# Kernel tuning notes

Measured on AMD Instinct MI355X. Metric: run time of the kernel, lower is better.

Reference implementation:

```python
import jax, jax.numpy as jnp
import numpy as np

NUM_HEAD = 8
GN_GROUPS = 32
EPS = 1e-5


def group_norm(x, w, b):
    # x: [B,C,H,W]; GroupNorm over 32 groups
    B, C, H, W = x.shape
    xg = x.reshape(B, GN_GROUPS, C // GN_GROUPS, H, W)
    mu = jnp.mean(xg, axis=(2, 3, 4), keepdims=True)
    var = jnp.var(xg, axis=(2, 3, 4), keepdims=True)
    xn = ((xg - mu) * jax.lax.rsqrt(var + EPS)).reshape(B, C, H, W)
    return xn * w[None, :, None, None] + b[None, :, None, None]


def conv1x1(x, w, b):
    # 1x1 conv == channel-wise linear: w [O,C], x [B,C,H,W]
    return jnp.einsum('oc,bchw->bohw', w, x) + b[None, :, None, None]


def setup_inputs() -> dict:
    key = jax.random.key(0)
    ks = jax.random.split(key, 6)
    B, C, H, W = 8, 512, 32, 32
    s = 1.0 / np.sqrt(C)
    return {
        'x': jax.random.normal(ks[0], (B, C, H, W), jnp.float32),
        'gn_w': jnp.ones((C,), jnp.float32),
        'gn_b': jnp.zeros((C,), jnp.float32),
        'wq': jax.random.normal(ks[1], (C, C), jnp.float32) * s,
        'bq': jnp.zeros((C,), jnp.float32),
        'wk': jax.random.normal(ks[2], (C, C), jnp.float32) * s,
        'bk': jnp.zeros((C,), jnp.float32),
        'wv': jax.random.normal(ks[3], (C, C), jnp.float32) * s,
        'bv': jnp.zeros((C,), jnp.float32),
        'wo': jax.random.normal(ks[4], (C, C), jnp.float32) * s,
        'bo': jnp.zeros((C,), jnp.float32),
    }


def reference(x, gn_w, gn_b, wq, bq, wk, bk, wv, bv, wo, bo):
    B, C, H, W = x.shape
    Hn = NUM_HEAD
    d = C // Hn
    N = H * W
    scale = d ** -0.5

    xn = group_norm(x, gn_w, gn_b)
    q = conv1x1(xn, wq, bq).reshape(B, Hn, d, N)  # [B,Hn,d,N]
    k = conv1x1(xn, wk, bk).reshape(B, Hn, d, N)
    v = conv1x1(xn, wv, bv).reshape(B, Hn, d, N)

    # attn[b,h,i,j] = sum_d q[b,h,d,i] * k[b,h,d,j]
    attn = jnp.einsum('bhdi,bhdj->bhij', q, k) * scale
    attn = jax.nn.softmax(attn, axis=-1)
    # out[b,h,d,i] = sum_j attn[b,h,i,j] * v[b,h,d,j]
    out = jnp.einsum('bhij,bhdj->bhdi', attn, v).reshape(B, C, H, W)
    return x + conv1x1(out, wo, bo)
```

## Files before the change

kernel.cpp:

```cpp
#include <hip/hip_runtime.h>
#include <hip/hip_bf16.h>

typedef unsigned short ushort_t;
typedef __bf16 bf16_t;
typedef bf16_t bf16x8 __attribute__((ext_vector_type(8)));
typedef float f32x4 __attribute__((ext_vector_type(4)));
typedef float f32x16 __attribute__((ext_vector_type(16)));

#define CH 512
#define NSP 1024

__device__ __forceinline__ float bf2f(ushort_t u) {
    union { unsigned int i; float f; } t; t.i = ((unsigned int)u) << 16; return t.f;
}
__device__ __forceinline__ ushort_t f2bf(float f) {
    union { float fl; unsigned int i; } t; t.fl = f;
    unsigned int r = t.i + 0x7fffu + ((t.i >> 16) & 1u);
    return (ushort_t)(r >> 16);
}
__device__ __forceinline__ unsigned int pk2(float a, float b) {
    __hip_bfloat162 h = __float22bfloat162_rn(make_float2(a, b));
    union { __hip_bfloat162 h2; unsigned int u; } t; t.h2 = h; return t.u;
}

#if __has_builtin(__builtin_amdgcn_global_load_lds)
#define HAVE_ASYNC_LDS 1
#endif
__device__ __forceinline__ void cp16(const ushort_t* g, ushort_t* l) {
#ifdef HAVE_ASYNC_LDS
    __builtin_amdgcn_global_load_lds((const __attribute__((address_space(1))) unsigned int*)g,
                                     (__attribute__((address_space(3))) unsigned int*)l, 16, 0, 0);
#else
    *(uint4*)l = *(const uint4*)g;
#endif
}

#if __has_builtin(__builtin_amdgcn_exp2f)
#define EXP2(x) __builtin_amdgcn_exp2f(x)
#else
#define EXP2(x) exp2f(x)
#endif

#define QSCALE 0.18033688011112042f

__global__ __launch_bounds__(256) void prep_w(const float* __restrict__ w0, const float* __restrict__ w1,
                                              const float* __restrict__ w2, const float* __restrict__ w3,
                                              ushort_t* __restrict__ wbf) {
    int idx = blockIdx.x * 256 + threadIdx.x;
    int my = idx >> 16;
    const float* src = (my == 0) ? w0 : (my == 1) ? w1 : (my == 2) ? w2 : w3;
    float4 v = reinterpret_cast<const float4*>(src)[idx & 65535];
    uint2 u = make_uint2(pk2(v.x, v.y), pk2(v.z, v.w));
    reinterpret_cast<uint2*>(wbf + (size_t)my * 262144)[idx & 65535] = u;
}

__global__ __launch_bounds__(256) void gn_fused(const float* __restrict__ x, const float* __restrict__ gw,
                                                const float* __restrict__ gbias,
                                                ushort_t* __restrict__ xnt) {
    __shared__ float red[8];
    int bg = blockIdx.x;
    int b = bg >> 5, g = bg & 31;
    int tid = threadIdx.x;
    const float4* x4 = reinterpret_cast<const float4*>(x + (size_t)bg * 16384);
    float4 v[16];
    float s = 0.f, s2 = 0.f;
    #pragma unroll
    for (int i = 0; i < 16; i++) {
        v[i] = x4[i * 256 + tid];
        s  += v[i].x + v[i].y + v[i].z + v[i].w;
        s2 += v[i].x * v[i].x + v[i].y * v[i].y + v[i].z * v[i].z + v[i].w * v[i].w;
    }
    #pragma unroll
    for (int off = 32; off > 0; off >>= 1) {
        s  += __shfl_down(s, off, 64);
        s2 += __shfl_down(s2, off, 64);
    }
    int wv = tid >> 6;
    if ((tid & 63) == 0) { red[wv] = s; red[4 + wv] = s2; }
    __syncthreads();
    float ts  = red[0] + red[1] + red[2] + red[3];
    float ts2 = red[4] + red[5] + red[6] + red[7];
    float mu  = ts * (1.f / 16384.f);
    float var = ts2 * (1.f / 16384.f) - mu * mu;
    float rstd = rsqrtf(var + 1e-5f);
    float ca[16], cb[16];
    #pragma unroll
    for (int cc = 0; cc < 16; cc++) {
        float ww = gw[g * 16 + cc], bb = gbias[g * 16 + cc];
        ca[cc] = rstd * ww; cb[cc] = bb - mu * ca[cc];
    }
    #pragma unroll
    for (int jj = 0; jj < 4; jj++) {
        float e[16];
        #pragma unroll
        for (int cc = 0; cc < 16; cc++) {
            float xv = (jj == 0) ? v[cc].x : (jj == 1) ? v[cc].y : (jj == 2) ? v[cc].z : v[cc].w;
            e[cc] = xv * ca[cc] + cb[cc];
        }
        uint4 u0 = make_uint4(pk2(e[0], e[1]), pk2(e[2], e[3]), pk2(e[4], e[5]), pk2(e[6], e[7]));
        uint4 u1 = make_uint4(pk2(e[8], e[9]), pk2(e[10], e[11]), pk2(e[12], e[13]), pk2(e[14], e[15]));
        ushort_t* dst = xnt + ((size_t)(b * 1024 + 4 * tid + jj)) * 512 + g * 16;
        *reinterpret_cast<uint4*>(dst)     = u0;
        *reinterpret_cast<uint4*>(dst + 8) = u1;
    }
}

__global__ __launch_bounds__(256) void conv_qkv(const ushort_t* __restrict__ xnt,
                                                const ushort_t* __restrict__ wbf,
                                                const float* __restrict__ bq,
                                                const float* __restrict__ bk,
                                                const float* __restrict__ bv,
                                                ushort_t* __restrict__ qt,
                                                ushort_t* __restrict__ kt,
                                                ushort_t* __restrict__ vt) {
    __shared__ __align__(16) char smem[17408];
// ... 51 lines not shown
        const float* bias = seg ? bk : bq;
        ushort_t* dst = seg ? kt : qt;
        float s = seg ? 1.f : QSCALE;
        float bv0 = bias[lo + wn * 32 + l15];
        float bv1 = bias[lo + wn * 32 + 16 + l15];
        ushort_t* cls = (ushort_t*)smem;
        #pragma unroll
        for (int ms = 0; ms < 4; ms++)
            #pragma unroll
            for (int ns = 0; ns < 2; ns++) {
                float bb = ns ? bv1 : bv0;
                int idx = (wm * 64 + ms * 16 + quad * 4) * 64 + wn * 32 + ns * 16 + l15;
                unsigned int ua = pk2((acc[ms][ns][0] + bb) * s, (acc[ms][ns][1] + bb) * s);
                unsigned int ub = pk2((acc[ms][ns][2] + bb) * s, (acc[ms][ns][3] + bb) * s);
                cls[idx]       = (ushort_t)(ua & 0xffff);
                cls[idx + 64]  = (ushort_t)(ua >> 16);
                cls[idx + 128] = (ushort_t)(ub & 0xffff);
                cls[idx + 192] = (ushort_t)(ub >> 16);
            }
        __syncthreads();
        int h = lo >> 6;
        size_t obase = ((size_t)(b * 8 + h) * 1024 + m0) * 64;
        #pragma unroll
        for (int rep = 0; rep < 4; rep++) {
            int id = rep * 256 + tid;
            int r = id >> 3, part = id & 7;
            *(uint4*)(dst + obase + (size_t)r * 64 + part * 8) = *(const uint4*)(cls + r * 64 + part * 8);
        }
    } else {
        float bv0 = bv[lo + wn * 32 + l15];
        float bv1 = bv[lo + wn * 32 + 16 + l15];
        ushort_t* clst = (ushort_t*)smem;
        #pragma unroll
        for (int ms = 0; ms < 4; ms++)
            #pragma unroll
            for (int ns = 0; ns < 2; ns++) {
                float bb = ns ? bv1 : bv0;
                unsigned int ua = pk2(acc[ms][ns][0] + bb, acc[ms][ns][1] + bb);
                unsigned int ub = pk2(acc[ms][ns][2] + bb, acc[ms][ns][3] + bb);
                *(uint2*)(&clst[(wn * 32 + ns * 16 + l15) * 136 + wm * 64 + ms * 16 + quad * 4]) =
                    make_uint2(ua, ub);
            }
        __syncthreads();
        #pragma unroll
        for (int rep = 0; rep < 4; rep++) {
            int id = rep * 256 + tid;
            int row = id >> 4, part = id & 15;
            *(uint4*)(vt + ((size_t)(b * 512 + lo + row) * 1024 + m0 + part * 8)) =
                *(const uint4*)(clst + row * 136 + part * 8);
        }
    }
}

#define Z16 {0.f,0.f,0.f,0.f,0.f,0.f,0.f,0.f,0.f,0.f,0.f,0.f,0.f,0.f,0.f,0.f}

#define PV_STEP(JS, P) {                                                                     \
    unsigned wA0 = pk2(P[((JS)&1)*8+0], P[((JS)&1)*8+1]);                                    \
    unsigned wA1 = pk2(P[((JS)&1)*8+2], P[((JS)&1)*8+3]);                                    \
    unsigned wB0 = pk2(P[((JS)&1)*8+4], P[((JS)&1)*8+5]);                                    \
    unsigned wB1 = pk2(P[((JS)&1)*8+6], P[((JS)&1)*8+7]);                                    \
    asm("v_permlane32_swap_b32 %0, %1" : "+v"(wA0), "+v"(wB0));                              \
    asm("v_permlane32_swap_b32 %0, %1" : "+v"(wA1), "+v"(wB1));                              \
    union { unsigned u[4]; bf16x8 v; } pa_;                                                  \
    pa_.u[0] = wA0; pa_.u[1] = wA1; pa_.u[2] = wB0; pa_.u[3] = wB1;                          \
    int phys_ = (((JS) * 2) | hi) ^ r7;                                                      \
    bf16x8 vf0 = *(const bf16x8*)(vbuf + l31 * 64 + phys_ * 8);                              \
    bf16x8 vf1 = *(const bf16x8*)(vbuf + (32 + l31) * 64 + phys_ * 8);                       \
    __builtin_amdgcn_s_setprio(1);                                                           \
    vacc0 = __builtin_amdgcn_mfma_f32_32x32x16_bf16(pa_.v, vf0, vacc0, 0, 0, 0);             \
    vacc1 = __builtin_amdgcn_mfma_f32_32x32x16_bf16(pa_.v, vf1, vacc1, 0, 0, 0);             \
    __builtin_amdgcn_s_setprio(0); }

__global__ __launch_bounds__(256) void attn_kernel(const ushort_t* __restrict__ qt,
                                                   const ushort_t* __restrict__ kt,
                                                   const ushort_t* __restrict__ vt,
                                                   ushort_t* __restrict__ ao) {
    __shared__ __align__(16) ushort_t smem[16384];
    int tid = threadIdx.x;
    int wave = tid >> 6, lane = tid & 63, l31 = lane & 31, hi = lane >> 5;
    int id = blockIdx.x;
    int bh = (id & 7) * 8 + (id >> 6);
    int i0 = ((id >> 3) & 7) * 128;
    const ushort_t* qb = qt + (size_t)bh * 65536;
    const ushort_t* kb = kt + (size_t)bh * 65536;
    const ushort_t* vb = vt + (size_t)bh * 65536;
    int iw0 = i0 + wave * 32;
    int r7 = l31 & 7;

    bf16x8 qf[4];
    #pragma unroll
    for (int ks = 0; ks < 4; ks++)
        qf[ks] = *(const bf16x8*)(qb + (size_t)(iw0 + l31) * 64 + ks * 16 + hi * 8);

    f32x16 vacc0 = Z16, vacc1 = Z16;
    float lacc = 0.f;

    int rk0 = tid >> 3, sk = tid & 7, rk1 = rk0 + 32;
    const ushort_t* kg0 = kb + rk0 * 64 + (sk ^ (rk0 & 7)) * 8;
    const ushort_t* kg1 = kb + rk1 * 64 + (sk ^ (rk1 & 7)) * 8;
    const ushort_t* vg0 = vb + (size_t)rk0 * 1024 + (sk ^ (rk0 & 7)) * 8;
    const ushort_t* vg1 = vb + (size_t)rk1 * 1024 + (sk ^ (rk1 & 7)) * 8;

    cp16(kg0, smem + tid * 8);
    cp16(kg1, smem + (tid + 256) * 8);
    cp16(vg0, smem + 8192 + tid * 8);
    cp16(vg1, smem + 8192 + (tid + 256) * 8);
    kg0 += 4096; kg1 += 4096; vg0 += 64; vg1 += 64;
    __syncthreads();

    for (int jt = 0; jt < 16; jt++) {
        int cur = jt & 1;
        if (jt < 15) {
            ushort_t* kd = smem + (cur ^ 1) * 4096;
            ushort_t* vd = smem + 8192 + (cur ^ 1) * 4096;
            cp16(kg0, kd + tid * 8);
            cp16(kg1, kd + (tid + 256) * 8);
            cp16(vg0, vd + tid * 8);
            cp16(vg1, vd + (tid + 256) * 8);
            kg0 += 4096; kg1 += 4096; vg0 += 64; vg1 += 64;
        }
        const ushort_t* kbuf = smem + cur * 4096;
        const ushort_t* vbuf = smem + 8192 + cur * 4096;

        f32x16 s0 = Z16, s1 = Z16;
        __builtin_amdgcn_s_setprio(1);
        #pragma unroll
        for (int ks = 0; ks < 4; ks++) {
            int phys = ((ks * 2) | hi) ^ r7;
            bf16x8 kf = *(const bf16x8*)(kbuf + l31 * 64 + phys * 8);
            s0 = __builtin_amdgcn_mfma_f32_32x32x16_bf16(kf, qf[ks], s0, 0, 0, 0);
        }
        #pragma unroll
        for (int ks = 0; ks < 4; ks++) {
            int phys = ((ks * 2) | hi) ^ r7;
            bf16x8 kf = *(const bf16x8*)(kbuf + (32 + l31) * 64 + phys * 8);
            s1 = __builtin_amdgcn_mfma_f32_32x32x16_bf16(kf, qf[ks], s1, 0, 0, 0);
        }
        __builtin_amdgcn_s_setprio(0);

        float p0[16], p1[16];
        #pragma unroll
        for (int r = 0; r < 16; r++) p0[r] = EXP2(s0[r]);
        #pragma unroll
        for (int r = 0; r < 16; r++) p1[r] = EXP2(s1[r]);
        float t0 = 0.f, t1 = 0.f, t2 = 0.f, t3 = 0.f;
        #pragma unroll
        for (int r = 0; r < 4; r++) { t0 += p0[r]; t1 += p0[4 + r]; t2 += p0[8 + r]; t3 += p0[12 + r]; }
        #pragma unroll
        for (int r = 0; r < 4; r++) { t0 += p1[r]; t1 += p1[4 + r]; t2 += p1[8 + r]; t3 += p1[12 + r]; }
        lacc += (t0 + t1) + (t2 + t3);

        PV_STEP(0, p0)
        PV_STEP(1, p0)
        PV_STEP(2, p1)
        PV_STEP(3, p1)

        __syncthreads();
    }

    lacc += __shfl_xor(lacc, 32, 64);
    float linv[16];
    #pragma unroll
    for (int r = 0; r < 16; r++) {
        int ir = (r & 3) + 8 * (r >> 2) + 4 * hi;
        linv[r] = 1.f / __shfl(lacc, ir, 64);
    }

    ushort_t* ols = smem;
    #pragma unroll
    for (int r = 0; r < 16; r++) {
        int irow = wave * 32 + (r & 3) + 8 * (r >> 2) + 4 * hi;
        ols[irow * 80 + l31]      = f2bf(vacc0[r] * linv[r]);
        ols[irow * 80 + 32 + l31] = f2bf(vacc1[r] * linv[r]);
    }
    __syncthreads();
    int b = bh >> 3, h = bh & 7;
    ushort_t* aob = ao + ((size_t)b * 1024 + i0) * 512 + h * 64;
    #pragma unroll
    for (int rep = 0; rep < 4; rep++) {
        int idd = rep * 256 + tid;
        int rl = idd >> 3, part = idd & 7;
        *(uint4*)(aob + (size_t)rl * 512 + part * 8) = *(const uint4*)(ols + rl * 80 + part * 8);
    }
}

__global__ __launch_bounds__(256) void conv_out(const ushort_t* __restrict__ ao,
                                                const ushort_t* __restrict__ wo,
                                                const float* __restrict__ bo,
                                                const float* __restrict__ xres,
                                                float* __restrict__ out) {
    __shared__ __align__(16) char smem[12288];
    ushort_t* als = (ushort_t*)smem;
    ushort_t* bls = (ushort_t*)(smem + 8192);
    int tid = threadIdx.x;
    int wave = tid >> 6, lane = tid & 63, l15 = lane & 15, quad = lane >> 4;
    int wm = wave >> 1, wn = wave & 1;
    int m0 = blockIdx.x * 128, o0 = blockIdx.y * 64, b = blockIdx.z;
    const ushort_t* A = ao + (size_t)b * 524288;

    f32x4 acc[4][2];
    #pragma unroll
    for (int ms = 0; ms < 4; ms++)
        #pragma unroll
        for (int ns = 0; ns < 2; ns++) acc[ms][ns] = (f32x4){0.f, 0.f, 0.f, 0.f};

    for (int k0 = 0; k0 < 512; k0 += 32) {
        #pragma unroll
        for (int rep = 0; rep < 2; rep++) {
            int id = rep * 256 + tid;
            int r = id >> 2, part = id & 3;
            int sw = part ^ ((r >> 2) & 3);
            cp16(A + (size_t)(m0 + r) * 512 + k0 + sw * 8, als + (size_t)id * 8);
        }
        {
            int r = tid >> 2, part = tid & 3;
            int sw = part ^ ((r >> 2) & 3);
            cp16(wo + (size_t)(o0 + r) * 512 + k0 + sw * 8, bls + (size_t)tid * 8);
        }
        __syncthreads();
        bf16x8 af[4], bfr[2];
        #pragma unroll
        for (int ms = 0; ms < 4; ms++) {
            int row = wm * 64 + ms * 16 + l15;
            int slot = quad ^ ((row >> 2) & 3);
            af[ms] = *(const bf16x8*)(als + row * 32 + slot * 8);
        }
        #pragma unroll
        for (int ns = 0; ns < 2; ns++) {
            int row = wn * 32 + ns * 16 + l15;
            int slot = quad ^ ((row >> 2) & 3);
            bfr[ns] = *(const bf16x8*)(bls + row * 32 + slot * 8);
        }
        #pragma unroll
        for (int ms = 0; ms < 4; ms++)
            #pragma unroll
            for (int ns = 0; ns < 2; ns++)
                acc[ms][ns] = __builtin_amdgcn_mfma_f32_16x16x32_bf16(af[ms], bfr[ns], acc[ms][ns], 0, 0, 0);
        __syncthreads();
    }

    #pragma unroll
    for (int ns = 0; ns < 2; ns++) {
        int o = o0 + wn * 32 + ns * 16 + l15;
        float bb = bo[o];
        #pragma unroll
        for (int ms = 0; ms < 4; ms++) {
            int n = m0 + wm * 64 + ms * 16 + quad * 4;
            size_t ga = ((size_t)(b * 512 + o)) * 1024 + n;
            float4 xv = *(const float4*)(xres + ga);
            float4 c4;
            c4.x = acc[ms][ns][0] + bb + xv.x;
            c4.y = acc[ms][ns][1] + bb + xv.y;
            c4.z = acc[ms][ns][2] + bb + xv.z;
            c4.w = acc[ms][ns][3] + bb + xv.w;
            *(float4*)(out + ga) = c4;
        }
    }
}

extern "C" void kernel_launch(void* const* d_in, const int* in_sizes, int n_in,
                              void* d_out, int out_size, void* d_ws, size_t ws_size,
                              hipStream_t stream) {
    const float* x    = (const float*)d_in[0];
    const float* gn_w = (const float*)d_in[1];
    const float* gn_b = (const float*)d_in[2];
    const float* wq   = (const float*)d_in[3];
    const float* bq   = (const float*)d_in[4];
    const float* wk   = (const float*)d_in[5];
    const float* bk   = (const float*)d_in[6];
    const float* wv   = (const float*)d_in[7];
    const float* bv   = (const float*)d_in[8];
    const float* wo   = (const float*)d_in[9];
    const float* bo   = (const float*)d_in[10];

    char* ws = (char*)d_ws;
    ushort_t* xnt  = (ushort_t*)(ws);
    ushort_t* qt   = (ushort_t*)(ws + (((size_t)8)  << 20));
    ushort_t* kt   = (ushort_t*)(ws + (((size_t)16) << 20));
    ushort_t* vt   = (ushort_t*)(ws + (((size_t)24) << 20));
    ushort_t* wbf  = (ushort_t*)(ws + (((size_t)32) << 20));
    ushort_t* ao   = xnt;

    prep_w<<<1024, 256, 0, stream>>>(wq, wk, wv, wo, wbf);
    gn_fused<<<256, 256, 0, stream>>>(x, gn_w, gn_b, xnt);

    conv_qkv<<<dim3(8, 24, 8), 256, 0, stream>>>(xnt, wbf, bq, bk, bv, qt, kt, vt);

    attn_kernel<<<512, 256, 0, stream>>>(qt, kt, vt, ao);

    conv_out<<<dim3(8, 8, 8), 256, 0, stream>>>(ao, wbf + 786432, bo, x, (float*)d_out);
}
```

Baseline: 159.9 us.

## Split attention key tiles across waves and halve query rows per block

Each attention block now processes 64 query rows with a 2x2 wave split over query rows and key halves, doubling the grid to 1024 blocks. Partial PV accumulators and row sums from the two key-half waves are reduced through shared memory before normalization and store. This is meant to raise parallelism and occupancy (with a launch-bounds hint of 4 blocks), at the cost of reloading K/V for twice as many blocks and an extra cross-wave reduction.

```diff
diff --git a/kernel.cpp b/kernel.cpp
--- a/kernel.cpp
+++ b/kernel.cpp
@@ -220,11 +220,11 @@
 
 #define Z16 {0.f,0.f,0.f,0.f,0.f,0.f,0.f,0.f,0.f,0.f,0.f,0.f,0.f,0.f,0.f,0.f}
 
-#define PV_STEP(JS, P) {                                                                     \
-    unsigned wA0 = pk2(P[((JS)&1)*8+0], P[((JS)&1)*8+1]);                                    \
-    unsigned wA1 = pk2(P[((JS)&1)*8+2], P[((JS)&1)*8+3]);                                    \
-    unsigned wB0 = pk2(P[((JS)&1)*8+4], P[((JS)&1)*8+5]);                                    \
-    unsigned wB1 = pk2(P[((JS)&1)*8+6], P[((JS)&1)*8+7]);                                    \
+#define PV_STEP(JS, PPTR) {                                                                  \
+    unsigned wA0 = pk2(PPTR[0], PPTR[1]);                                                    \
+    unsigned wA1 = pk2(PPTR[2], PPTR[3]);                                                    \
+    unsigned wB0 = pk2(PPTR[4], PPTR[5]);                                                    \
+    unsigned wB1 = pk2(PPTR[6], PPTR[7]);                                                    \
     asm("v_permlane32_swap_b32 %0, %1" : "+v"(wA0), "+v"(wB0));                              \
     asm("v_permlane32_swap_b32 %0, %1" : "+v"(wA1), "+v"(wB1));                              \
     union { unsigned u[4]; bf16x8 v; } pa_;                                                  \
@@ -237,21 +237,24 @@
     vacc1 = __builtin_amdgcn_mfma_f32_32x32x16_bf16(pa_.v, vf1, vacc1, 0, 0, 0);             \
     __builtin_amdgcn_s_setprio(0); }
 
-__global__ __launch_bounds__(256) void attn_kernel(const ushort_t* __restrict__ qt,
-                                                   const ushort_t* __restrict__ kt,
-                                                   const ushort_t* __restrict__ vt,
-                                                   ushort_t* __restrict__ ao) {
+__global__ __launch_bounds__(256, 4) void attn_kernel(const ushort_t* __restrict__ qt,
+                                                      const ushort_t* __restrict__ kt,
+                                                      const ushort_t* __restrict__ vt,
+                                                      ushort_t* __restrict__ ao) {
     __shared__ __align__(16) ushort_t smem[16384];
+    __shared__ float lred[128];
     int tid = threadIdx.x;
     int wave = tid >> 6, lane = tid & 63, l31 = lane & 31, hi = lane >> 5;
+    int wi = wave & 1, wj = wave >> 1;
     int id = blockIdx.x;
-    int bh = (id & 7) * 8 + (id >> 6);
-    int i0 = ((id >> 3) & 7) * 128;
+    int bh = (id & 7) * 8 + (id >> 7);
+    int i0 = ((id >> 3) & 15) * 64;
     const ushort_t* qb = qt + (size_t)bh * 65536;
     const ushort_t* kb = kt + (size_t)bh * 65536;
     const ushort_t* vb = vt + (size_t)bh * 65536;
-    int iw0 = i0 + wave * 32;
+    int iw0 = i0 + wi * 32;
     int r7 = l31 & 7;
+    int jrow = wj * 32 + l31;
 
     bf16x8 qf[4];
     #pragma unroll
@@ -288,62 +291,66 @@
         const ushort_t* kbuf = smem + cur * 4096;
         const ushort_t* vbuf = smem + 8192 + cur * 4096;
 
-        f32x16 s0 = Z16, s1 = Z16;
+        f32x16 s = Z16;
         __builtin_amdgcn_s_setprio(1);
         #pragma unroll
         for (int ks = 0; ks < 4; ks++) {
             int phys = ((ks * 2) | hi) ^ r7;
-            bf16x8 kf = *(const bf16x8*)(kbuf + l31 * 64 + phys * 8);
-            s0 = __builtin_amdgcn_mfma_f32_32x32x16_bf16(kf, qf[ks], s0, 0, 0, 0);
-        }
-        #pragma unroll
-        for (int ks = 0; ks < 4; ks++) {
-            int phys = ((ks * 2) | hi) ^ r7;
-            bf16x8 kf = *(const bf16x8*)(kbuf + (32 + l31) * 64 + phys * 8);
-            s1 = __builtin_amdgcn_mfma_f32_32x32x16_bf16(kf, qf[ks], s1, 0, 0, 0);
+            bf16x8 kf = *(const bf16x8*)(kbuf + jrow * 64 + phys * 8);
+            s = __builtin_amdgcn_mfma_f32_32x32x16_bf16(kf, qf[ks], s, 0, 0, 0);
         }
         __builtin_amdgcn_s_setprio(0);
 
-        float p0[16], p1[16];
-        #pragma unroll
-        for (int r = 0; r < 16; r++) p0[r] = EXP2(s0[r]);
-        #pragma unroll
-        for (int r = 0; r < 16; r++) p1[r] = EXP2(s1[r]);
+        float p[16];
+        #pragma unroll
+        for (int r = 0; r < 16; r++) p[r] = EXP2(s[r]);
         float t0 = 0.f, t1 = 0.f, t2 = 0.f, t3 = 0.f;
         #pragma unroll
-        for (int r = 0; r < 4; r++) { t0 += p0[r]; t1 += p0[4 + r]; t2 += p0[8 + r]; t3 += p0[12 + r]; }
-        #pragma unroll
-        for (int r = 0; r < 4; r++) { t0 += p1[r]; t1 += p1[4 + r]; t2 += p1[8 + r]; t3 += p1[12 + r]; }
+        for (int r = 0; r < 4; r++) { t0 += p[r]; t1 += p[4 + r]; t2 += p[8 + r]; t3 += p[12 + r]; }
         lacc += (t0 + t1) + (t2 + t3);
 
-        PV_STEP(0, p0)
-        PV_STEP(1, p0)
-        PV_STEP(2, p1)
-        PV_STEP(3, p1)
+        PV_STEP(wj * 2,     (p))
+        PV_STEP(wj * 2 + 1, (p + 8))
 
         __syncthreads();
     }
 
     lacc += __shfl_xor(lacc, 32, 64);
-    float linv[16];
-    #pragma unroll
-    for (int r = 0; r < 16; r++) {
-        int ir = (r & 3) + 8 * (r >> 2) + 4 * hi;
-        linv[r] = 1.f / __shfl(lacc, ir, 64);
-    }
-
-    ushort_t* ols = smem;
-    #pragma unroll
-    for (int r = 0; r < 16; r++) {
-        int irow = wave * 32 + (r & 3) + 8 * (r >> 2) + 4 * hi;
-        ols[irow * 80 + l31]      = f2bf(vacc0[r] * linv[r]);
-        ols[irow * 80 + 32 + l31] = f2bf(vacc1[r] * linv[r]);
+    lred[wave * 32 + l31] = lacc;
+
+    float* om = (float*)smem;
+    if (wj == 1) {
+        #pragma unroll
+        for (int r = 0; r < 16; r++) {
+            int row = wi * 32 + (r & 3) + 8 * (r >> 2) + 4 * hi;
+            om[row * 64 + l31]      = vacc0[r];
+            om[row * 64 + 32 + l31] = vacc1[r];
+        }
+    }
+    __syncthreads();
+    ushort_t* ols = smem + 8192;
+    if (wj == 0) {
+        float ltot = lacc + lred[(wave ^ 2) * 32 + l31];
+        float linv[16];
+        #pragma unroll
+        for (int r = 0; r < 16; r++) {
+            int ir = (r & 3) + 8 * (r >> 2) + 4 * hi;
+            linv[r] = 1.f / __shfl(ltot, ir, 64);
+        }
+        #pragma unroll
+        for (int r = 0; r < 16; r++) {
+            int row = wi * 32 + (r & 3) + 8 * (r >> 2) + 4 * hi;
+            float o0 = vacc0[r] + om[row * 64 + l31];
+            float o1 = vacc1[r] + om[row * 64 + 32 + l31];
+            ols[row * 80 + l31]      = f2bf(o0 * linv[r]);
+            ols[row * 80 + 32 + l31] = f2bf(o1 * linv[r]);
+        }
     }
     __syncthreads();
     int b = bh >> 3, h = bh & 7;
     ushort_t* aob = ao + ((size_t)b * 1024 + i0) * 512 + h * 64;
     #pragma unroll
-    for (int rep = 0; rep < 4; rep++) {
+    for (int rep = 0; rep < 2; rep++) {
         int idd = rep * 256 + tid;
         int rl = idd >> 3, part = idd & 7;
         *(uint4*)(aob + (size_t)rl * 512 + part * 8) = *(const uint4*)(ols + rl * 80 + part * 8);
@@ -452,7 +459,7 @@
 
     conv_qkv<<<dim3(8, 24, 8), 256, 0, stream>>>(xnt, wbf, bq, bk, bv, qt, kt, vt);
 
-    attn_kernel<<<512, 256, 0, stream>>>(qt, kt, vt, ao);
+    attn_kernel<<<1024, 256, 0, stream>>>(qt, kt, vt, ao);
 
     conv_out<<<dim3(8, 8, 8), 256, 0, stream>>>(ao, wbf + 786432, bo, x, (float*)d_out);
 }
```

Result: no change. 160.1 us (+0.1%).

## Split attention KV tile across wave pairs with 64-row query tiles per wave

Applied to the files above, without the earlier changes.

Each wave now handles 64 query rows against half of each 64-key tile, rather than 32 query rows against the full tile. Every K and V fragment read from LDS is therefore reused across two MFMAs, which cuts LDS read traffic per MFMA. The two partial outputs and row sums are combined through shared memory at the end. In exchange, accumulator register pressure doubles, a cross-wave reduction with extra barriers is added, and launch bounds request two blocks per CU.

```diff
diff --git a/kernel.cpp b/kernel.cpp
--- a/kernel.cpp
+++ b/kernel.cpp
@@ -220,46 +220,57 @@
 
 #define Z16 {0.f,0.f,0.f,0.f,0.f,0.f,0.f,0.f,0.f,0.f,0.f,0.f,0.f,0.f,0.f,0.f}
 
-#define PV_STEP(JS, P) {                                                                     \
-    unsigned wA0 = pk2(P[((JS)&1)*8+0], P[((JS)&1)*8+1]);                                    \
-    unsigned wA1 = pk2(P[((JS)&1)*8+2], P[((JS)&1)*8+3]);                                    \
-    unsigned wB0 = pk2(P[((JS)&1)*8+4], P[((JS)&1)*8+5]);                                    \
-    unsigned wB1 = pk2(P[((JS)&1)*8+6], P[((JS)&1)*8+7]);                                    \
-    asm("v_permlane32_swap_b32 %0, %1" : "+v"(wA0), "+v"(wB0));                              \
-    asm("v_permlane32_swap_b32 %0, %1" : "+v"(wA1), "+v"(wB1));                              \
-    union { unsigned u[4]; bf16x8 v; } pa_;                                                  \
-    pa_.u[0] = wA0; pa_.u[1] = wA1; pa_.u[2] = wB0; pa_.u[3] = wB1;                          \
+#define PV_STEP2(JS, PA, PB) {                                                               \
+    unsigned a0 = pk2(PA[0], PA[1]), a1 = pk2(PA[2], PA[3]);                                 \
+    unsigned a2 = pk2(PA[4], PA[5]), a3 = pk2(PA[6], PA[7]);                                 \
+    asm("v_permlane32_swap_b32 %0, %1" : "+v"(a0), "+v"(a2));                                \
+    asm("v_permlane32_swap_b32 %0, %1" : "+v"(a1), "+v"(a3));                                \
+    union { unsigned u[4]; bf16x8 v; } paA_;                                                 \
+    paA_.u[0] = a0; paA_.u[1] = a1; paA_.u[2] = a2; paA_.u[3] = a3;                          \
+    unsigned b0 = pk2(PB[0], PB[1]), b1 = pk2(PB[2], PB[3]);                                 \
+    unsigned b2 = pk2(PB[4], PB[5]), b3 = pk2(PB[6], PB[7]);                                 \
+    asm("v_permlane32_swap_b32 %0, %1" : "+v"(b0), "+v"(b2));                                \
+    asm("v_permlane32_swap_b32 %0, %1" : "+v"(b1), "+v"(b3));                                \
+    union { unsigned u[4]; bf16x8 v; } paB_;                                                 \
+    paB_.u[0] = b0; paB_.u[1] = b1; paB_.u[2] = b2; paB_.u[3] = b3;                          \
     int phys_ = (((JS) * 2) | hi) ^ r7;                                                      \
     bf16x8 vf0 = *(const bf16x8*)(vbuf + l31 * 64 + phys_ * 8);                              \
     bf16x8 vf1 = *(const bf16x8*)(vbuf + (32 + l31) * 64 + phys_ * 8);                       \
     __builtin_amdgcn_s_setprio(1);                                                           \
-    vacc0 = __builtin_amdgcn_mfma_f32_32x32x16_bf16(pa_.v, vf0, vacc0, 0, 0, 0);             \
-    vacc1 = __builtin_amdgcn_mfma_f32_32x32x16_bf16(pa_.v, vf1, vacc1, 0, 0, 0);             \
+    vacc0A = __builtin_amdgcn_mfma_f32_32x32x16_bf16(paA_.v, vf0, vacc0A, 0, 0, 0);          \
+    vacc1A = __builtin_amdgcn_mfma_f32_32x32x16_bf16(paA_.v, vf1, vacc1A, 0, 0, 0);          \
+    vacc0B = __builtin_amdgcn_mfma_f32_32x32x16_bf16(paB_.v, vf0, vacc0B, 0, 0, 0);          \
+    vacc1B = __builtin_amdgcn_mfma_f32_32x32x16_bf16(paB_.v, vf1, vacc1B, 0, 0, 0);          \
     __builtin_amdgcn_s_setprio(0); }
 
-__global__ __launch_bounds__(256) void attn_kernel(const ushort_t* __restrict__ qt,
-                                                   const ushort_t* __restrict__ kt,
-                                                   const ushort_t* __restrict__ vt,
-                                                   ushort_t* __restrict__ ao) {
+__global__ __launch_bounds__(256, 2) void attn_kernel(const ushort_t* __restrict__ qt,
+                                                      const ushort_t* __restrict__ kt,
+                                                      const ushort_t* __restrict__ vt,
+                                                      ushort_t* __restrict__ ao) {
     __shared__ __align__(16) ushort_t smem[16384];
+    __shared__ float lred[256];
     int tid = threadIdx.x;
     int wave = tid >> 6, lane = tid & 63, l31 = lane & 31, hi = lane >> 5;
+    int wi = wave & 1, wj = wave >> 1;
     int id = blockIdx.x;
     int bh = (id & 7) * 8 + (id >> 6);
     int i0 = ((id >> 3) & 7) * 128;
     const ushort_t* qb = qt + (size_t)bh * 65536;
     const ushort_t* kb = kt + (size_t)bh * 65536;
     const ushort_t* vb = vt + (size_t)bh * 65536;
-    int iw0 = i0 + wave * 32;
+    int iw0 = i0 + wi * 64;
     int r7 = l31 & 7;
-
-    bf16x8 qf[4];
-    #pragma unroll
-    for (int ks = 0; ks < 4; ks++)
-        qf[ks] = *(const bf16x8*)(qb + (size_t)(iw0 + l31) * 64 + ks * 16 + hi * 8);
-
-    f32x16 vacc0 = Z16, vacc1 = Z16;
-    float lacc = 0.f;
+    int jrow = wj * 32 + l31;
+
+    bf16x8 qfA[4], qfB[4];
+    #pragma unroll
+    for (int ks = 0; ks < 4; ks++) {
+        qfA[ks] = *(const bf16x8*)(qb + (size_t)(iw0 + l31) * 64 + ks * 16 + hi * 8);
+        qfB[ks] = *(const bf16x8*)(qb + (size_t)(iw0 + 32 + l31) * 64 + ks * 16 + hi * 8);
+    }
+
+    f32x16 vacc0A = Z16, vacc1A = Z16, vacc0B = Z16, vacc1B = Z16;
+    float laccA = 0.f, laccB = 0.f;
 
     int rk0 = tid >> 3, sk = tid & 7, rk1 = rk0 + 32;
     const ushort_t* kg0 = kb + rk0 * 64 + (sk ^ (rk0 & 7)) * 8;
@@ -288,56 +299,84 @@
         const ushort_t* kbuf = smem + cur * 4096;
         const ushort_t* vbuf = smem + 8192 + cur * 4096;
 
-        f32x16 s0 = Z16, s1 = Z16;
+        f32x16 sA = Z16, sB = Z16;
         __builtin_amdgcn_s_setprio(1);
         #pragma unroll
         for (int ks = 0; ks < 4; ks++) {
             int phys = ((ks * 2) | hi) ^ r7;
-            bf16x8 kf = *(const bf16x8*)(kbuf + l31 * 64 + phys * 8);
-            s0 = __builtin_amdgcn_mfma_f32_32x32x16_bf16(kf, qf[ks], s0, 0, 0, 0);
-        }
-        #pragma unroll
-        for (int ks = 0; ks < 4; ks++) {
-            int phys = ((ks * 2) | hi) ^ r7;
-            bf16x8 kf = *(const bf16x8*)(kbuf + (32 + l31) * 64 + phys * 8);
-            s1 = __builtin_amdgcn_mfma_f32_32x32x16_bf16(kf, qf[ks], s1, 0, 0, 0);
+            bf16x8 kf = *(const bf16x8*)(kbuf + jrow * 64 + phys * 8);
+            sA = __builtin_amdgcn_mfma_f32_32x32x16_bf16(kf, qfA[ks], sA, 0, 0, 0);
+            sB = __builtin_amdgcn_mfma_f32_32x32x16_bf16(kf, qfB[ks], sB, 0, 0, 0);
         }
         __builtin_amdgcn_s_setprio(0);
 
-        float p0[16], p1[16];
-        #pragma unroll
-        for (int r = 0; r < 16; r++) p0[r] = EXP2(s0[r]);
-        #pragma unroll
-        for (int r = 0; r < 16; r++) p1[r] = EXP2(s1[r]);
-        float t0 = 0.f, t1 = 0.f, t2 = 0.f, t3 = 0.f;
-        #pragma unroll
-        for (int r = 0; r < 4; r++) { t0 += p0[r]; t1 += p0[4 + r]; t2 += p0[8 + r]; t3 += p0[12 + r]; }
-        #pragma unroll
-        for (int r = 0; r < 4; r++) { t0 += p1[r]; t1 += p1[4 + r]; t2 += p1[8 + r]; t3 += p1[12 + r]; }
-        lacc += (t0 + t1) + (t2 + t3);
-
-        PV_STEP(0, p0)
-        PV_STEP(1, p0)
-        PV_STEP(2, p1)
-        PV_STEP(3, p1)
-
-        __syncthreads();
-    }
-
-    lacc += __shfl_xor(lacc, 32, 64);
-    float linv[16];
-    #pragma unroll
-    for (int r = 0; r < 16; r++) {
-        int ir = (r & 3) + 8 * (r >> 2) + 4 * hi;
-        linv[r] = 1.f / __shfl(lacc, ir, 64);
-    }
-
+        float pA[16], pB[16];
+        #pragma unroll
+        for (int r = 0; r < 16; r++) pA[r] = EXP2(sA[r]);
+        #pragma unroll
+        for (int r = 0; r < 16; r++) pB[r] = EXP2(sB[r]);
+        {
+            float t0 = 0.f, t1 = 0.f, t2 = 0.f, t3 = 0.f;
+            #pragma unroll
+            for (int r = 0; r < 4; r++) { t0 += pA[r]; t1 += pA[4 + r]; t2 += pA[8 + r]; t3 += pA[12 + r]; }
+            laccA += (t0 + t1) + (t2 + t3);
+        }
+        {
+            float t0 = 0.f, t1 = 0.f, t2 = 0.f, t3 = 0.f;
+            #pragma unroll
+            for (int r = 0; r < 4; r++) { t0 += pB[r]; t1 += pB[4 + r]; t2 += pB[8 + r]; t3 += pB[12 + r]; }
+            laccB += (t0 + t1) + (t2 + t3);
+        }
+
+        PV_STEP2(wj * 2,     (pA),     (pB))
+        PV_STEP2(wj * 2 + 1, (pA + 8), (pB + 8))
+
+        __syncthreads();
+    }
+
+    laccA += __shfl_xor(laccA, 32, 64);
+    laccB += __shfl_xor(laccB, 32, 64);
+    lred[wave * 64 + l31]      = laccA;
+    lred[wave * 64 + 32 + l31] = laccB;
+
+    float* om = (float*)smem;
+    if (wj == 1) {
+        #pragma unroll
+        for (int r = 0; r < 16; r++) {
+            int crow = (r & 3) + 8 * (r >> 2) + 4 * hi;
+            om[(wi * 64 + crow) * 64 + l31]           = vacc0A[r];
+            om[(wi * 64 + crow) * 64 + 32 + l31]      = vacc1A[r];
+            om[(wi * 64 + 32 + crow) * 64 + l31]      = vacc0B[r];
+            om[(wi * 64 + 32 + crow) * 64 + 32 + l31] = vacc1B[r];
+        }
+    }
+    __syncthreads();
+    float oa0[16], oa1[16], ob0[16], ob1[16];
+    if (wj == 0) {
+        float ltA = laccA + lred[(wave ^ 2) * 64 + l31];
+        float ltB = laccB + lred[(wave ^ 2) * 64 + 32 + l31];
+        #pragma unroll
+        for (int r = 0; r < 16; r++) {
+            int ir = (r & 3) + 8 * (r >> 2) + 4 * hi;
+            float lA = 1.f / __shfl(ltA, ir, 64);
+            float lB = 1.f / __shfl(ltB, ir, 64);
+            oa0[r] = (vacc0A[r] + om[(wi * 64 + ir) * 64 + l31])           * lA;
+            oa1[r] = (vacc1A[r] + om[(wi * 64 + ir) * 64 + 32 + l31])      * lA;
+            ob0[r] = (vacc0B[r] + om[(wi * 64 + 32 + ir) * 64 + l31])      * lB;
+            ob1[r] = (vacc1B[r] + om[(wi * 64 + 32 + ir) * 64 + 32 + l31]) * lB;
+        }
+    }
+    __syncthreads();
     ushort_t* ols = smem;
-    #pragma unroll
-    for (int r = 0; r < 16; r++) {
-        int irow = wave * 32 + (r & 3) + 8 * (r >> 2) + 4 * hi;
-        ols[irow * 80 + l31]      = f2bf(vacc0[r] * linv[r]);
-        ols[irow * 80 + 32 + l31] = f2bf(vacc1[r] * linv[r]);
+    if (wj == 0) {
+        #pragma unroll
+        for (int r = 0; r < 16; r++) {
+            int ir = (r & 3) + 8 * (r >> 2) + 4 * hi;
+            ols[(wi * 64 + ir) * 80 + l31]           = f2bf(oa0[r]);
+            ols[(wi * 64 + ir) * 80 + 32 + l31]      = f2bf(oa1[r]);
+            ols[(wi * 64 + 32 + ir) * 80 + l31]      = f2bf(ob0[r]);
+            ols[(wi * 64 + 32 + ir) * 80 + 32 + l31] = f2bf(ob1[r]);
+        }
     }
     __syncthreads();
     int b = bh >> 3, h = bh & 7;
```

Result: slower. 163.4 us (+2.2%).

## Fuse all stages into one cooperative persistent kernel with grid syncs

Applied to the files above, without the earlier changes.

Replaces the five separate launches (weight prep, group norm, QKV conv, attention, output conv) with a single cooperative kernel of 512 blocks that walks the stages and separates them with grid.sync. The aim is to remove per-launch overhead and the gaps between kernels. The fallback path also merges weight prep and group norm into one kernel. The cost is grid-wide barriers, uneven stage work (1280 and 1536 virtual blocks over 512 blocks), and launch_bounds(256,2) register limits applied to every stage, including attention.

```diff
diff --git a/kernel.cpp b/kernel.cpp
--- a/kernel.cpp
+++ b/kernel.cpp
@@ -1,5 +1,8 @@
 #include <hip/hip_runtime.h>
 #include <hip/hip_bf16.h>
+#include <hip/hip_cooperative_groups.h>
+
+namespace cg = cooperative_groups;
 
 typedef unsigned short ushort_t;
 typedef __bf16 bf16_t;
@@ -43,24 +46,44 @@
 
 #define QSCALE 0.18033688011112042f
 
-__global__ __launch_bounds__(256) void prep_w(const float* __restrict__ w0, const float* __restrict__ w1,
-                                              const float* __restrict__ w2, const float* __restrict__ w3,
-                                              ushort_t* __restrict__ wbf) {
-    int idx = blockIdx.x * 256 + threadIdx.x;
-    int my = idx >> 16;
-    const float* src = (my == 0) ? w0 : (my == 1) ? w1 : (my == 2) ? w2 : w3;
-    float4 v = reinterpret_cast<const float4*>(src)[idx & 65535];
-    uint2 u = make_uint2(pk2(v.x, v.y), pk2(v.z, v.w));
-    reinterpret_cast<uint2*>(wbf + (size_t)my * 262144)[idx & 65535] = u;
-}
-
-__global__ __launch_bounds__(256) void gn_fused(const float* __restrict__ x, const float* __restrict__ gw,
-                                                const float* __restrict__ gbias,
-                                                ushort_t* __restrict__ xnt) {
+#define Z16 {0.f,0.f,0.f,0.f,0.f,0.f,0.f,0.f,0.f,0.f,0.f,0.f,0.f,0.f,0.f,0.f}
+
+#define PV_STEP(JS, P) {                                                                     \
+    unsigned wA0 = pk2(P[((JS)&1)*8+0], P[((JS)&1)*8+1]);                                    \
+    unsigned wA1 = pk2(P[((JS)&1)*8+2], P[((JS)&1)*8+3]);                                    \
+    unsigned wB0 = pk2(P[((JS)&1)*8+4], P[((JS)&1)*8+5]);                                    \
+    unsigned wB1 = pk2(P[((JS)&1)*8+6], P[((JS)&1)*8+7]);                                    \
+    asm("v_permlane32_swap_b32 %0, %1" : "+v"(wA0), "+v"(wB0));                              \
+    asm("v_permlane32_swap_b32 %0, %1" : "+v"(wA1), "+v"(wB1));                              \
+    union { unsigned u[4]; bf16x8 v; } pa_;                                                  \
+    pa_.u[0] = wA0; pa_.u[1] = wA1; pa_.u[2] = wB0; pa_.u[3] = wB1;                          \
+    int phys_ = (((JS) * 2) | hi) ^ r7;                                                      \
+    bf16x8 vf0 = *(const bf16x8*)(vbuf + l31 * 64 + phys_ * 8);                              \
+    bf16x8 vf1 = *(const bf16x8*)(vbuf + (32 + l31) * 64 + phys_ * 8);                       \
+    __builtin_amdgcn_s_setprio(1);                                                           \
+    vacc0 = __builtin_amdgcn_mfma_f32_32x32x16_bf16(pa_.v, vf0, vacc0, 0, 0, 0);             \
+    vacc1 = __builtin_amdgcn_mfma_f32_32x32x16_bf16(pa_.v, vf1, vacc1, 0, 0, 0);             \
+    __builtin_amdgcn_s_setprio(0); }
+
+
+__global__ __launch_bounds__(256) void prep_gn(const float* __restrict__ x, const float* __restrict__ gw,
+                                               const float* __restrict__ gbias,
+                                               const float* __restrict__ w0, const float* __restrict__ w1,
+                                               const float* __restrict__ w2, const float* __restrict__ w3,
+                                               ushort_t* __restrict__ wbf, ushort_t* __restrict__ xnt) {
+    int tid = threadIdx.x;
+    if (blockIdx.x >= 256) {
+        int idx = (blockIdx.x - 256) * 256 + tid;
+        int my = idx >> 16;
+        const float* src = (my == 0) ? w0 : (my == 1) ? w1 : (my == 2) ? w2 : w3;
+        float4 v = reinterpret_cast<const float4*>(src)[idx & 65535];
+        uint2 u = make_uint2(pk2(v.x, v.y), pk2(v.z, v.w));
+        reinterpret_cast<uint2*>(wbf + (size_t)my * 262144)[idx & 65535] = u;
+        return;
+    }
     __shared__ float red[8];
     int bg = blockIdx.x;
     int b = bg >> 5, g = bg & 31;
-    int tid = threadIdx.x;
     const float4* x4 = reinterpret_cast<const float4*>(x + (size_t)bg * 16384);
     float4 v[16];
     float s = 0.f, s2 = 0.f;
@@ -218,25 +241,6 @@
     }
 }
 
-#define Z16 {0.f,0.f,0.f,0.f,0.f,0.f,0.f,0.f,0.f,0.f,0.f,0.f,0.f,0.f,0.f,0.f}
-
-#define PV_STEP(JS, P) {                                                                     \
-    unsigned wA0 = pk2(P[((JS)&1)*8+0], P[((JS)&1)*8+1]);                                    \
-    unsigned wA1 = pk2(P[((JS)&1)*8+2], P[((JS)&1)*8+3]);                                    \
-    unsigned wB0 = pk2(P[((JS)&1)*8+4], P[((JS)&1)*8+5]);                                    \
-    unsigned wB1 = pk2(P[((JS)&1)*8+6], P[((JS)&1)*8+7]);                                    \
-    asm("v_permlane32_swap_b32 %0, %1" : "+v"(wA0), "+v"(wB0));                              \
-    asm("v_permlane32_swap_b32 %0, %1" : "+v"(wA1), "+v"(wB1));                              \
-    union { unsigned u[4]; bf16x8 v; } pa_;                                                  \
-    pa_.u[0] = wA0; pa_.u[1] = wA1; pa_.u[2] = wB0; pa_.u[3] = wB1;                          \
-    int phys_ = (((JS) * 2) | hi) ^ r7;                                                      \
-    bf16x8 vf0 = *(const bf16x8*)(vbuf + l31 * 64 + phys_ * 8);                              \
-    bf16x8 vf1 = *(const bf16x8*)(vbuf + (32 + l31) * 64 + phys_ * 8);                       \
-    __builtin_amdgcn_s_setprio(1);                                                           \
-    vacc0 = __builtin_amdgcn_mfma_f32_32x32x16_bf16(pa_.v, vf0, vacc0, 0, 0, 0);             \
-    vacc1 = __builtin_amdgcn_mfma_f32_32x32x16_bf16(pa_.v, vf1, vacc1, 0, 0, 0);             \
-    __builtin_amdgcn_s_setprio(0); }
-
 __global__ __launch_bounds__(256) void attn_kernel(const ushort_t* __restrict__ qt,
                                                    const ushort_t* __restrict__ kt,
                                                    const ushort_t* __restrict__ vt,
@@ -424,6 +428,370 @@
     }
 }
 
+__global__ __launch_bounds__(256, 2) void fused_all(
+    const float* __restrict__ x, const float* __restrict__ gnw, const float* __restrict__ gnb,
+    const float* __restrict__ wq, const float* __restrict__ bq,
+    const float* __restrict__ wk, const float* __restrict__ bk,
+    const float* __restrict__ wv, const float* __restrict__ bv,
+    const float* __restrict__ wo, const float* __restrict__ bo,
+    ushort_t* __restrict__ xnt, ushort_t* __restrict__ qt, ushort_t* __restrict__ kt,
+    ushort_t* __restrict__ vt, ushort_t* __restrict__ wbf, float* __restrict__ out)
+{
+    cg::grid_group grid = cg::this_grid();
+    __shared__ __align__(16) char SMEM[32768];
+    int tid = threadIdx.x;
+    int bid = blockIdx.x;
+    ushort_t* ao = xnt;
+
+    for (int vb = bid; vb < 1280; vb += 512) {
+        if (vb >= 256) {
+            int idx = (vb - 256) * 256 + tid;
+            int my = idx >> 16;
+            const float* src = (my == 0) ? wq : (my == 1) ? wk : (my == 2) ? wv : wo;
+            float4 v = reinterpret_cast<const float4*>(src)[idx & 65535];
+            uint2 u = make_uint2(pk2(v.x, v.y), pk2(v.z, v.w));
+            reinterpret_cast<uint2*>(wbf + (size_t)my * 262144)[idx & 65535] = u;
+        } else {
+            float* red = (float*)SMEM;
+            int bg = vb, b = bg >> 5, g = bg & 31;
+            const float4* x4 = reinterpret_cast<const float4*>(x + (size_t)bg * 16384);
+            float4 v[16];
+            float s = 0.f, s2 = 0.f;
+            #pragma unroll
+            for (int i = 0; i < 16; i++) {
+                v[i] = x4[i * 256 + tid];
+                s  += v[i].x + v[i].y + v[i].z + v[i].w;
+                s2 += v[i].x * v[i].x + v[i].y * v[i].y + v[i].z * v[i].z + v[i].w * v[i].w;
+            }
+            #pragma unroll
+            for (int off = 32; off > 0; off >>= 1) {
+                s  += __shfl_down(s, off, 64);
+                s2 += __shfl_down(s2, off, 64);
+            }
+            int wv_ = tid >> 6;
+            if ((tid & 63) == 0) { red[wv_] = s; red[4 + wv_] = s2; }
+            __syncthreads();
+            float ts  = red[0] + red[1] + red[2] + red[3];
+            float ts2 = red[4] + red[5] + red[6] + red[7];
+            float mu  = ts * (1.f / 16384.f);
+            float var = ts2 * (1.f / 16384.f) - mu * mu;
+            float rstd = rsqrtf(var + 1e-5f);
+            float ca[16], cb[16];
+            #pragma unroll
+            for (int cc = 0; cc < 16; cc++) {
+                float ww = gnw[g * 16 + cc], bb = gnb[g * 16 + cc];
+                ca[cc] = rstd * ww; cb[cc] = bb - mu * ca[cc];
+            }
+            #pragma unroll
+            for (int jj = 0; jj < 4; jj++) {
+                float e[16];
+                #pragma unroll
+                for (int cc = 0; cc < 16; cc++) {
+                    float xv = (jj == 0) ? v[cc].x : (jj == 1) ? v[cc].y : (jj == 2) ? v[cc].z : v[cc].w;
+                    e[cc] = xv * ca[cc] + cb[cc];
+                }
+                uint4 u0 = make_uint4(pk2(e[0], e[1]), pk2(e[2], e[3]), pk2(e[4], e[5]), pk2(e[6], e[7]));
+                uint4 u1 = make_uint4(pk2(e[8], e[9]), pk2(e[10], e[11]), pk2(e[12], e[13]), pk2(e[14], e[15]));
+                ushort_t* dst = xnt + ((size_t)(b * 1024 + 4 * tid + jj)) * 512 + g * 16;
+                *reinterpret_cast<uint4*>(dst)     = u0;
+                *reinterpret_cast<uint4*>(dst + 8) = u1;
+            }
+            __syncthreads();
+        }
+    }
+    __threadfence();
+    grid.sync();
+
+    for (int vb = bid; vb < 1536; vb += 512) {
+        int m0 = (vb & 7) * 128, o0 = ((vb >> 3) % 24) * 64, b = vb / 192;
+        ushort_t* als = (ushort_t*)SMEM;
+        ushort_t* bls = (ushort_t*)(SMEM + 8192);
+        int wave = tid >> 6, lane = tid & 63, l15 = lane & 15, quad = lane >> 4;
+        int wm = wave >> 1, wn = wave & 1;
+        const ushort_t* A = xnt + (size_t)b * 524288;
+
+        f32x4 acc[4][2];
+        #pragma unroll
+        for (int ms = 0; ms < 4; ms++)
+            #pragma unroll
+            for (int ns = 0; ns < 2; ns++) acc[ms][ns] = (f32x4){0.f, 0.f, 0.f, 0.f};
+
+        __syncthreads();
+        for (int k0 = 0; k0 < 512; k0 += 32) {
+            #pragma unroll
+            for (int rep = 0; rep < 2; rep++) {
+                int id = rep * 256 + tid;
+                int r = id >> 2, part = id & 3;
+                int sw = part ^ ((r >> 2) & 3);
+                cp16(A + (size_t)(m0 + r) * 512 + k0 + sw * 8, als + (size_t)id * 8);
+            }
+            {
+                int r = tid >> 2, part = tid & 3;
+                int sw = part ^ ((r >> 2) & 3);
+                cp16(wbf + (size_t)(o0 + r) * 512 + k0 + sw * 8, bls + (size_t)tid * 8);
+            }
+            __syncthreads();
+            bf16x8 af[4], bfr[2];
+            #pragma unroll
+            for (int ms = 0; ms < 4; ms++) {
+                int row = wm * 64 + ms * 16 + l15;
+                int slot = quad ^ ((row >> 2) & 3);
+                af[ms] = *(const bf16x8*)(als + row * 32 + slot * 8);
+            }
+            #pragma unroll
+            for (int ns = 0; ns < 2; ns++) {
+                int row = wn * 32 + ns * 16 + l15;
+                int slot = quad ^ ((row >> 2) & 3);
+                bfr[ns] = *(const bf16x8*)(bls + row * 32 + slot * 8);
+            }
+            #pragma unroll
+            for (int ms = 0; ms < 4; ms++)
+                #pragma unroll
+                for (int ns = 0; ns < 2; ns++)
+                    acc[ms][ns] = __builtin_amdgcn_mfma_f32_16x16x32_bf16(af[ms], bfr[ns], acc[ms][ns], 0, 0, 0);
+            __syncthreads();
+        }
+
+        int seg = o0 >> 9, lo = o0 & 511;
+        if (seg < 2) {
+            const float* bias = seg ? bk : bq;
+            ushort_t* dst = seg ? kt : qt;
+            float s = seg ? 1.f : QSCALE;
+            float bv0 = bias[lo + wn * 32 + l15];
+            float bv1 = bias[lo + wn * 32 + 16 + l15];
+            ushort_t* cls = (ushort_t*)SMEM;
+            #pragma unroll
+            for (int ms = 0; ms < 4; ms++)
+                #pragma unroll
+                for (int ns = 0; ns < 2; ns++) {
+                    float bb = ns ? bv1 : bv0;
+                    int idx = (wm * 64 + ms * 16 + quad * 4) * 64 + wn * 32 + ns * 16 + l15;
+                    unsigned int ua = pk2((acc[ms][ns][0] + bb) * s, (acc[ms][ns][1] + bb) * s);
+                    unsigned int ub = pk2((acc[ms][ns][2] + bb) * s, (acc[ms][ns][3] + bb) * s);
+                    cls[idx]       = (ushort_t)(ua & 0xffff);
+                    cls[idx + 64]  = (ushort_t)(ua >> 16);
+                    cls[idx + 128] = (ushort_t)(ub & 0xffff);
+                    cls[idx + 192] = (ushort_t)(ub >> 16);
+                }
+            __syncthreads();
+            int h = lo >> 6;
+            size_t obase = ((size_t)(b * 8 + h) * 1024 + m0) * 64;
+            #pragma unroll
+            for (int rep = 0; rep < 4; rep++) {
+                int id = rep * 256 + tid;
+                int r = id >> 3, part = id & 7;
+                *(uint4*)(dst + obase + (size_t)r * 64 + part * 8) = *(const uint4*)(cls + r * 64 + part * 8);
+            }
+        } else {
+            float bv0 = bv[lo + wn * 32 + l15];
+            float bv1 = bv[lo + wn * 32 + 16 + l15];
+            ushort_t* clst = (ushort_t*)SMEM;
+            #pragma unroll
+            for (int ms = 0; ms < 4; ms++)
+                #pragma unroll
+                for (int ns = 0; ns < 2; ns++) {
+                    float bb = ns ? bv1 : bv0;
+                    unsigned int ua = pk2(acc[ms][ns][0] + bb, acc[ms][ns][1] + bb);
+                    unsigned int ub = pk2(acc[ms][ns][2] + bb, acc[ms][ns][3] + bb);
+                    *(uint2*)(&clst[(wn * 32 + ns * 16 + l15) * 136 + wm * 64 + ms * 16 + quad * 4]) =
+                        make_uint2(ua, ub);
+                }
+            __syncthreads();
+            #pragma unroll
+            for (int rep = 0; rep < 4; rep++) {
+                int id = rep * 256 + tid;
+                int row = id >> 4, part = id & 15;
+                *(uint4*)(vt + ((size_t)(b * 512 + lo + row) * 1024 + m0 + part * 8)) =
+                    *(const uint4*)(clst + row * 136 + part * 8);
+            }
+        }
+        __syncthreads();
+    }
+    __threadfence();
+    grid.sync();
+
+    {
+        ushort_t* smem = (ushort_t*)SMEM;
+        int wave = tid >> 6, lane = tid & 63, l31 = lane & 31, hi = lane >> 5;
+        int id = bid;
+        int bh = (id & 7) * 8 + (id >> 6);
+        int i0 = ((id >> 3) & 7) * 128;
+        const ushort_t* qb = qt + (size_t)bh * 65536;
+        const ushort_t* kb = kt + (size_t)bh * 65536;
+        const ushort_t* vb2 = vt + (size_t)bh * 65536;
+        int iw0 = i0 + wave * 32;
+        int r7 = l31 & 7;
+
+        bf16x8 qf[4];
+        #pragma unroll
+        for (int ks = 0; ks < 4; ks++)
+            qf[ks] = *(const bf16x8*)(qb + (size_t)(iw0 + l31) * 64 + ks * 16 + hi * 8);
+
+        f32x16 vacc0 = Z16, vacc1 = Z16;
+        float lacc = 0.f;
+
+        int rk0 = tid >> 3, sk = tid & 7, rk1 = rk0 + 32;
+        const ushort_t* kg0 = kb + rk0 * 64 + (sk ^ (rk0 & 7)) * 8;
+        const ushort_t* kg1 = kb + rk1 * 64 + (sk ^ (rk1 & 7)) * 8;
+        const ushort_t* vg0 = vb2 + (size_t)rk0 * 1024 + (sk ^ (rk0 & 7)) * 8;
+        const ushort_t* vg1 = vb2 + (size_t)rk1 * 1024 + (sk ^ (rk1 & 7)) * 8;
+
+        cp16(kg0, smem + tid * 8);
+        cp16(kg1, smem + (tid + 256) * 8);
+        cp16(vg0, smem + 8192 + tid * 8);
+        cp16(vg1, smem + 8192 + (tid + 256) * 8);
+        kg0 += 4096; kg1 += 4096; vg0 += 64; vg1 += 64;
+        __syncthreads();
+
+        for (int jt = 0; jt < 16; jt++) {
+            int cur = jt & 1;
+            if (jt < 15) {
+                ushort_t* kd = smem + (cur ^ 1) * 4096;
+                ushort_t* vd = smem + 8192 + (cur ^ 1) * 4096;
+                cp16(kg0, kd + tid * 8);
+                cp16(kg1, kd + (tid + 256) * 8);
+                cp16(vg0, vd + tid * 8);
+                cp16(vg1, vd + (tid + 256) * 8);
+                kg0 += 4096; kg1 += 4096; vg0 += 64; vg1 += 64;
+            }
+            const ushort_t* kbuf = smem + cur * 4096;
+            const ushort_t* vbuf = smem + 8192 + cur * 4096;
+
+            f32x16 s0 = Z16, s1 = Z16;
+            __builtin_amdgcn_s_setprio(1);
+            #pragma unroll
+            for (int ks = 0; ks < 4; ks++) {
+                int phys = ((ks * 2) | hi) ^ r7;
+                bf16x8 kf = *(const bf16x8*)(kbuf + l31 * 64 + phys * 8);
+                s0 = __builtin_amdgcn_mfma_f32_32x32x16_bf16(kf, qf[ks], s0, 0, 0, 0);
+            }
+            #pragma unroll
+            for (int ks = 0; ks < 4; ks++) {
+                int phys = ((ks * 2) | hi) ^ r7;
+                bf16x8 kf = *(const bf16x8*)(kbuf + (32 + l31) * 64 + phys * 8);
+                s1 = __builtin_amdgcn_mfma_f32_32x32x16_bf16(kf, qf[ks], s1, 0, 0, 0);
+            }
+            __builtin_amdgcn_s_setprio(0);
+
+            float p0[16], p1[16];
+            #pragma unroll
+            for (int r = 0; r < 16; r++) p0[r] = EXP2(s0[r]);
+            #pragma unroll
+            for (int r = 0; r < 16; r++) p1[r] = EXP2(s1[r]);
+            float t0 = 0.f, t1 = 0.f, t2 = 0.f, t3 = 0.f;
+            #pragma unroll
+            for (int r = 0; r < 4; r++) { t0 += p0[r]; t1 += p0[4 + r]; t2 += p0[8 + r]; t3 += p0[12 + r]; }
+            #pragma unroll
+            for (int r = 0; r < 4; r++) { t0 += p1[r]; t1 += p1[4 + r]; t2 += p1[8 + r]; t3 += p1[12 + r]; }
+            lacc += (t0 + t1) + (t2 + t3);
+
+            PV_STEP(0, p0)
+            PV_STEP(1, p0)
+            PV_STEP(2, p1)
+            PV_STEP(3, p1)
+
+            __syncthreads();
+        }
+
+        lacc += __shfl_xor(lacc, 32, 64);
+        float linv[16];
+        #pragma unroll
+        for (int r = 0; r < 16; r++) {
+            int ir = (r & 3) + 8 * (r >> 2) + 4 * hi;
+            linv[r] = 1.f / __shfl(lacc, ir, 64);
+        }
+
+        ushort_t* ols = smem;
+        #pragma unroll
+        for (int r = 0; r < 16; r++) {
+            int irow = wave * 32 + (r & 3) + 8 * (r >> 2) + 4 * hi;
+            ols[irow * 80 + l31]      = f2bf(vacc0[r] * linv[r]);
+            ols[irow * 80 + 32 + l31] = f2bf(vacc1[r] * linv[r]);
+        }
+        __syncthreads();
+        int b = bh >> 3, h = bh & 7;
+        ushort_t* aob = ao + ((size_t)b * 1024 + i0) * 512 + h * 64;
+        #pragma unroll
+        for (int rep = 0; rep < 4; rep++) {
+            int idd = rep * 256 + tid;
+            int rl = idd >> 3, part = idd & 7;
+            *(uint4*)(aob + (size_t)rl * 512 + part * 8) = *(const uint4*)(ols + rl * 80 + part * 8);
+        }
+    }
+    __threadfence();
+    grid.sync();
+
+    {
+        int m0 = (bid & 7) * 128, o0 = ((bid >> 3) & 7) * 64, b = bid >> 6;
+        ushort_t* als = (ushort_t*)SMEM;
+        ushort_t* bls = (ushort_t*)(SMEM + 8192);
+        const ushort_t* wob = wbf + 786432;
+        int wave = tid >> 6, lane = tid & 63, l15 = lane & 15, quad = lane >> 4;
+        int wm = wave >> 1, wn = wave & 1;
+        const ushort_t* A = ao + (size_t)b * 524288;
+
+        f32x4 acc[4][2];
+        #pragma unroll
+        for (int ms = 0; ms < 4; ms++)
+            #pragma unroll
+            for (int ns = 0; ns < 2; ns++) acc[ms][ns] = (f32x4){0.f, 0.f, 0.f, 0.f};
+
+        __syncthreads();
+        for (int k0 = 0; k0 < 512; k0 += 32) {
+            #pragma unroll
+            for (int rep = 0; rep < 2; rep++) {
+                int id = rep * 256 + tid;
+                int r = id >> 2, part = id & 3;
+                int sw = part ^ ((r >> 2) & 3);
+                cp16(A + (size_t)(m0 + r) * 512 + k0 + sw * 8, als + (size_t)id * 8);
+            }
+            {
+                int r = tid >> 2, part = tid & 3;
+                int sw = part ^ ((r >> 2) & 3);
+                cp16(wob + (size_t)(o0 + r) * 512 + k0 + sw * 8, bls + (size_t)tid * 8);
+            }
+            __syncthreads();
+            bf16x8 af[4], bfr[2];
+            #pragma unroll
+            for (int ms = 0; ms < 4; ms++) {
+                int row = wm * 64 + ms * 16 + l15;
+                int slot = quad ^ ((row >> 2) & 3);
+                af[ms] = *(const bf16x8*)(als + row * 32 + slot * 8);
+            }
+            #pragma unroll
+            for (int ns = 0; ns < 2; ns++) {
+                int row = wn * 32 + ns * 16 + l15;
+                int slot = quad ^ ((row >> 2) & 3);
+                bfr[ns] = *(const bf16x8*)(bls + row * 32 + slot * 8);
+            }
+            #pragma unroll
+            for (int ms = 0; ms < 4; ms++)
+                #pragma unroll
+                for (int ns = 0; ns < 2; ns++)
+                    acc[ms][ns] = __builtin_amdgcn_mfma_f32_16x16x32_bf16(af[ms], bfr[ns], acc[ms][ns], 0, 0, 0);
+            __syncthreads();
+        }
+
+        #pragma unroll
+        for (int ns = 0; ns < 2; ns++) {
+            int o = o0 + wn * 32 + ns * 16 + l15;
+            float bb = bo[o];
+            #pragma unroll
+            for (int ms = 0; ms < 4; ms++) {
+                int n = m0 + wm * 64 + ms * 16 + quad * 4;
+                size_t ga = ((size_t)(b * 512 + o)) * 1024 + n;
+                float4 xv = *(const float4*)(x + ga);
+                float4 c4;
+                c4.x = acc[ms][ns][0] + bb + xv.x;
+                c4.y = acc[ms][ns][1] + bb + xv.y;
+                c4.z = acc[ms][ns][2] + bb + xv.z;
+                c4.w = acc[ms][ns][3] + bb + xv.w;
+                *(float4*)(out + ga) = c4;
+            }
+        }
+    }
+}
+
 extern "C" void kernel_launch(void* const* d_in, const int* in_sizes, int n_in,
                               void* d_out, int out_size, void* d_ws, size_t ws_size,
                               hipStream_t stream) {
@@ -445,14 +813,21 @@
     ushort_t* kt   = (ushort_t*)(ws + (((size_t)16) << 20));
     ushort_t* vt   = (ushort_t*)(ws + (((size_t)24) << 20));
     ushort_t* wbf  = (ushort_t*)(ws + (((size_t)32) << 20));
-    ushort_t* ao   = xnt;
-
-    prep_w<<<1024, 256, 0, stream>>>(wq, wk, wv, wo, wbf);
-    gn_fused<<<256, 256, 0, stream>>>(x, gn_w, gn_b, xnt);
-
-    conv_qkv<<<dim3(8, 24, 8), 256, 0, stream>>>(xnt, wbf, bq, bk, bv, qt, kt, vt);
-
-    attn_kernel<<<512, 256, 0, stream>>>(qt, kt, vt, ao);
-
-    conv_out<<<dim3(8, 8, 8), 256, 0, stream>>>(ao, wbf + 786432, bo, x, (float*)d_out);
-}
+    float* outp = (float*)d_out;
+    ushort_t* ao = xnt;
+
+    void* args[] = {
+        (void*)&x, (void*)&gn_w, (void*)&gn_b,
+        (void*)&wq, (void*)&bq, (void*)&wk, (void*)&bk,
+        (void*)&wv, (void*)&bv, (void*)&wo, (void*)&bo,
+        (void*)&xnt, (void*)&qt, (void*)&kt, (void*)&vt, (void*)&wbf, (void*)&outp
+    };
+    hipError_t err = hipLaunchCooperativeKernel((void*)fused_all, dim3(512), dim3(256),
+                                                args, 0, stream);
+    if (err != hipSuccess) {
+        prep_gn<<<1280, 256, 0, stream>>>(x, gn_w, gn_b, wq, wk, wv, wo, wbf, xnt);
+        conv_qkv<<<dim3(8, 24, 8), 256, 0, stream>>>(xnt, wbf, bq, bk, bv, qt, kt, vt);
+        attn_kernel<<<512, 256, 0, stream>>>(qt, kt, vt, ao);
+        conv_out<<<dim3(8, 8, 8), 256, 0, stream>>>(ao, wbf + 786432, bo, x, outp);
+    }
+}
```

Result: slower. 508.1 us (+217.7%).
